# Kernel optimization log

Hardware: AMD Instinct MI355X
Metric: run time of the kernel (lower is better)

The kernel has to match this reference:

```python
import math
import jax, jax.numpy as jnp
import numpy as np

LN_2PI = math.log(2.0 * math.pi)


def _patches(x, K, s):
    # x: (N,1,h,w) -> (N,K*K,oh,ow); channel i*K+j is the (i,j)-shifted strided slice
    N, _, h, w = x.shape
    oh = (h - K) // s + 1
    ow = (w - K) // s + 1
    cols = [x[:, 0, i:i + s * (oh - 1) + 1:s, j:j + s * (ow - 1) + 1:s]
            for i in range(K) for j in range(K)]
    return jnp.stack(cols, axis=1)


def _em_routing(a, V, beta_a, beta_u, max_iter, C):
    # a: (b,ni,nj), V: (b,ni,nj,16)
    b, ni, nj, _ = V.shape
    ba = jnp.tile(beta_a, nj // C)[None, None, :]            # (1,1,nj)
    bu = jnp.tile(beta_u, nj // C)[None, None, :, None]      # (1,1,nj,1)
    R = jnp.full((b, ni, nj), 1.0 / nj, dtype=V.dtype)
    a_out = None
    miu = None
    for t in range(max_iter):
        lam = 0.01 * (1.0 - 0.95 ** (t + 1))
        R4 = (R * a)[..., None]                              # (b,ni,nj,1)
        coeff = jnp.maximum(R4.sum(1, keepdims=True), 1e-8)  # (b,1,nj,1)
        R4 = R4 / coeff
        miu = (R4 * V).sum(1, keepdims=True)                 # (b,1,nj,16)
        d2 = (V - miu) ** 2
        sigma = jnp.maximum((R4 * d2).sum(1, keepdims=True), 1e-8)
        log_sigma = jnp.log(sigma)
        cost = (bu + 0.5 * log_sigma) * coeff                # (b,1,nj,16)
        a_out = jax.nn.sigmoid(lam * (ba - cost.sum(-1)))    # (b,1,nj)
        if t != max_iter - 1:
            logp = -0.5 * (LN_2PI + log_sigma + d2 / sigma).sum(-1)  # (b,ni,nj)
            R = jax.nn.softmax(a_out * logp, axis=-1)
    return a_out[:, 0], miu[:, 0]


def _conv_capsule(a, M, W, beta_a, beta_u, B, C, K, stride, iters,
                  share=False, add_coord=False):
    bB, _, h, w = a.shape
    b = bB // B
    oh = (h - K) // stride + 1
    ow = (w - K) // stride + 1
    KK = K * K
    # pose patches -> (b,B,KK,1,oh*ow,4,4)
    Mp = _patches(M, K, stride).reshape(b, B, 4, 4, KK, 1, oh * ow)
    Mp = jnp.transpose(Mp, (0, 1, 4, 5, 6, 2, 3))
    if share:
        V = W[None, :, None, :, None] @ Mp                   # (b,B,KK,C,ohw,4,4)
    else:
        V = W[None, :, :, :, None] @ Mp
    if add_coord:
        ii = np.repeat(np.arange(K), K).astype(np.float32)
        jj = np.tile(np.arange(K), K).astype(np.float32)
        ll = np.repeat(np.arange(oh), ow).astype(np.float32)
        kk = np.tile(np.arange(ow), oh).astype(np.float32)
        pos_x = (stride * kk[None, :] + ii[:, None]) / w
        pos_y = (stride * ll[None, :] + jj[:, None]) / h
        coords = jnp.asarray(np.stack([pos_x, pos_y], -1))   # (KK,ohw,2)
        V = V.at[:, :, :, :, :, 0, :2].add(coords[None, None, :, None, :, :].astype(V.dtype))
    ap = _patches(a, K, stride).reshape(b, B * KK, oh * ow)
    a_i = jnp.tile(ap, (1, 1, C))                            # (b,B*KK,C*ohw)
    Vf = V.reshape(b, B * KK, C * oh * ow, 16)
    a_j, M_j = _em_routing(a_i, Vf, beta_a, beta_u, iters, C)
    a_out = a_j.reshape(b * C, 1, oh, ow)
    # faithful to original: permute(0,2,1) then flat view -> (b*C*16,1,oh,ow)
    M_out = jnp.transpose(M_j, (0, 2, 1)).reshape(b * C * 16, 1, oh, ow)
    return a_out, M_out


def setup_inputs() -> dict:
    key = jax.random.key(0)
    ks = jax.random.split(key, 16)
    f32 = jnp.float32
    eye = jnp.eye(4, dtype=f32)
    inp = {
        "x": jax.random.normal(ks[0], (16, 2, 32, 32), dtype=f32),
        "conv_w": 0.015 * jax.random.normal(ks[1], (32, 2, 5, 5), dtype=f32),
        "conv_b": jnp.zeros((32,), dtype=f32),
        "pose_w": 0.01 * jax.random.normal(ks[2], (512, 32), dtype=f32),
        "pose_b": jnp.zeros((512,), dtype=f32),
        "act_w": 0.01 * jax.random.normal(ks[3], (32, 32), dtype=f32),
        "act_b": jnp.zeros((32,), dtype=f32),
        "W2": eye[None, None] + jax.random.uniform(ks[4], (32, 9, 32, 4, 4), dtype=f32, minval=-0.03, maxval=0.03),
        "beta_a2": 0.1 * jax.random.normal(ks[5], (32,), dtype=f32),
        "beta_u2": 0.1 * jax.random.normal(ks[6], (32,), dtype=f32),
        "W3": eye[None, None] + jax.random.uniform(ks[7], (32, 9, 32, 4, 4), dtype=f32, minval=-0.03, maxval=0.03),
        "beta_a3": 0.1 * jax.random.normal(ks[8], (32,), dtype=f32),
        "beta_u3": 0.1 * jax.random.normal(ks[9], (32,), dtype=f32),
        "W4": eye[None] + jax.random.uniform(ks[10], (32, 5, 4, 4), dtype=f32, minval=-0.03, maxval=0.03),
        "beta_a4": 0.1 * jax.random.normal(ks[11], (5,), dtype=f32),
        "beta_u4": 0.1 * jax.random.normal(ks[12], (5,), dtype=f32),
    }
    return inp


def reference(x, conv_w, conv_b, pose_w, pose_b, act_w, act_b,
              W2, beta_a2, beta_u2, W3, beta_a3, beta_u3, W4, beta_a4, beta_u4):
    # stem conv 5x5 stride 2 + relu: (b,2,32,32) -> (b,32,14,14)
    fea = jax.lax.conv_general_dilated(
        x, conv_w, window_strides=(2, 2), padding="VALID",
        dimension_numbers=("NCHW", "OIHW", "NCHW")) + conv_b[None, :, None, None]
    fea = jax.nn.relu(fea)
    # primary capsules (1x1 convs)
    M = jnp.einsum("bchw,oc->bohw", fea, pose_w) + pose_b[None, :, None, None]
    a = jax.nn.sigmoid(jnp.einsum("bchw,oc->bohw", fea, act_w) + act_b[None, :, None, None])
    bsz, _, h, w = a.shape
    a = a.reshape(-1, 1, h, w)      # (b*32,1,14,14)
    M = M.reshape(-1, 1, h, w)      # (b*512,1,14,14)
    a, M = _conv_capsule(a, M, W2, beta_a2, beta_u2, B=32, C=32, K=3, stride=2, iters=3)
    a, M = _conv_capsule(a, M, W3, beta_a3, beta_u3, B=32, C=32, K=3, stride=1, iters=3)
    a, _ = _conv_capsule(a, M, W4, beta_a4, beta_u4, B=32, C=5, K=4, stride=1, iters=3,
                         share=True, add_coord=True)
    return a.reshape(x.shape[0], 5)
```

## Files before the change

kernel.cpp:

```cpp
#include <hip/hip_runtime.h>
#include <math.h>

#define LN2PI 1.83787706640934548356f

__global__ void k_stem(const float* __restrict__ x, const float* __restrict__ w,
                       const float* __restrict__ bias, float* __restrict__ fea) {
    int idx = blockIdx.x * blockDim.x + threadIdx.x;
    if (idx >= 16*32*14*14) return;
    int ox = idx % 14, oy = (idx/14) % 14, oc = (idx/196) % 32, b = idx/(196*32);
    float s = bias[oc];
    const float* xb = x + b*2*1024;
    const float* wc = w + oc*2*25;
    #pragma unroll
    for (int ic = 0; ic < 2; ++ic)
        #pragma unroll
        for (int ky = 0; ky < 5; ++ky)
            #pragma unroll
            for (int kx = 0; kx < 5; ++kx)
                s = fmaf(xb[ic*1024 + (oy*2+ky)*32 + (ox*2+kx)],
                         wc[ic*25 + ky*5 + kx], s);
    fea[idx] = fmaxf(s, 0.f);
}

__global__ void k_primary(const float* __restrict__ fea,
                          const float* __restrict__ pw, const float* __restrict__ pb,
                          const float* __restrict__ aw, const float* __restrict__ ab,
                          float* __restrict__ M, float* __restrict__ a) {
    int idx = blockIdx.x * blockDim.x + threadIdx.x;
    if (idx >= 16*544*196) return;
    int hw = idx % 196, o = (idx/196) % 544, b = idx/(196*544);
    const float* f = fea + b*32*196 + hw;
    if (o < 512) {
        float s = pb[o];
        #pragma unroll
        for (int c = 0; c < 32; ++c) s = fmaf(f[c*196], pw[o*32+c], s);
        M[(b*512+o)*196 + hw] = s;
    } else {
        int oo = o - 512;
        float s = ab[oo];
        #pragma unroll
        for (int c = 0; c < 32; ++c) s = fmaf(f[c*196], aw[oo*32+c], s);
        a[(b*32+oo)*196 + hw] = 1.f/(1.f + __expf(-s));
    }
}

__global__ void k_patch(const float* __restrict__ a_in, const float* __restrict__ M_in,
                        float* __restrict__ aP, float4* __restrict__ MpV,
                        int B, int K, int stride, int h, int w, int oh, int ow) {
    int P = oh*ow, KK = K*K, ni = B*KK;
    int idx = blockIdx.x * blockDim.x + threadIdx.x;
    if (idx >= 16*ni*P) return;
    int i = idx % ni, p = (idx/ni) % P, b = idx/(ni*P);
    int Bi = i / KK, kk = i % KK, ki = kk / K, kj = kk % K;
    int py = p / ow, px = p % ow;
    int src = (py*stride + ki)*w + (px*stride + kj);
    int hw = h*w;
    aP[idx] = a_in[(b*B + Bi)*hw + src];
    const float* Ms = M_in + (size_t)((b*B + Bi)*16)*hw + src;
    size_t base = (size_t)(b*P + p)*4;
    #pragma unroll
    for (int m4 = 0; m4 < 4; ++m4)
        MpV[(base + m4)*ni + i] = make_float4(Ms[(4*m4+0)*hw], Ms[(4*m4+1)*hw],
                                              Ms[(4*m4+2)*hw], Ms[(4*m4+3)*hw]);
}

__global__ void k_wt(const float* __restrict__ W, float4* __restrict__ WtV,
                     int NI, int C) {
    int idx = blockIdx.x * blockDim.x + threadIdx.x;
    if (idx >= NI*C) return;
    int i = idx % NI, c = idx/NI;
    const float* src = W + (size_t)(i*C + c)*16;
    #pragma unroll
    for (int m4 = 0; m4 < 4; ++m4)
        WtV[((size_t)c*4 + m4)*NI + i] = make_float4(src[4*m4+0], src[4*m4+1],
                                                     src[4*m4+2], src[4*m4+3]);
}

template<int NI, int NJ, int P, int C>
__global__ __launch_bounds__(256)
void k_stats(const float* __restrict__ aP, const float4* __restrict__ MpV,
             const float4* __restrict__ WtV, const float* __restrict__ svb,
             const float* __restrict__ mxs, const float* __restrict__ ism,
             const float* __restrict__ beta_a, const float* __restrict__ beta_u,
             float* __restrict__ statP,
             float* __restrict__ a_fin, float* __restrict__ M_fin,
             int t, float lam, int fin)
{
    constexpr int NIT = (NI + 63) / 64;
    constexpr int RS = 20;
    __shared__ float sRed[4][33*RS];
    int wave = threadIdx.x >> 6, lane = threadIdx.x & 63;
    int g  = blockIdx.x % (16*P);
    int cg = blockIdx.x / (16*P);
    int c  = cg*4 + wave;
    int bb = g / P, p = g % P;
    int j  = c*P + p;

    const float*  aPb = aP  + (size_t)(bb*P + p)*NI;
    const float4* Mb  = MpV + (size_t)(bb*P + p)*4*NI;
    const float4* Wb  = WtV + (size_t)c*4*NI;
    const float*  svr = svb + (size_t)(bb*NJ + j)*NI;
    const float*  mxb = mxs + bb*NI;
    const float*  imb = ism + bb*NI;

    float accw = 0.f, accm[16], acc2[16];
    #pragma unroll
    for (int m = 0; m < 16; ++m) { accm[m] = 0.f; acc2[m] = 0.f; }

    for (int it = 0; it < NIT; ++it) {
        int i = lane + it*64;
        if ((NI % 64 == 0) || (i < NI)) {
            float r;
            if (t == 0) r = 1.f / NJ;
            else        r = __expf(svr[i] - mxb[i]) * imb[i];
            float wgt = r * aPb[i];
            float4 m0 = Mb[0*NI + i], m1 = Mb[1*NI + i];
            float4 m2 = Mb[2*NI + i], m3 = Mb[3*NI + i];
            accw += wgt;
            #pragma unroll
            for (int rr = 0; rr < 4; ++rr) {
                float4 w = Wb[rr*NI + i];
                float v0 = fmaf(w.w, m3.x, fmaf(w.z, m2.x, fmaf(w.y, m1.x, w.x*m0.x)));
                float v1 = fmaf(w.w, m3.y, fmaf(w.z, m2.y, fmaf(w.y, m1.y, w.x*m0.y)));
                float v2 = fmaf(w.w, m3.z, fmaf(w.z, m2.z, fmaf(w.y, m1.z, w.x*m0.z)));
                float v3 = fmaf(w.w, m3.w, fmaf(w.z, m2.w, fmaf(w.y, m1.w, w.x*m0.w)));
                float t0 = wgt*v0, t1 = wgt*v1, t2 = wgt*v2, t3 = wgt*v3;
                accm[rr*4+0] += t0; acc2[rr*4+0] = fmaf(t0, v0, acc2[rr*4+0]);
                accm[rr*4+1] += t1; acc2[rr*4+1] = fmaf(t1, v1, acc2[rr*4+1]);
                accm[rr*4+2] += t2; acc2[rr*4+2] = fmaf(t2, v2, acc2[rr*4+2]);
                accm[rr*4+3] += t3; acc2[rr*4+3] = fmaf(t3, v3, acc2[rr*4+3]);
            }
        }
    }

    accw += __shfl_xor(accw, 1); accw += __shfl_xor(accw, 2);
    #pragma unroll
    for (int m = 0; m < 16; ++m) {
        accm[m] += __shfl_xor(accm[m], 1); accm[m] += __shfl_xor(accm[m], 2);
        acc2[m] += __shfl_xor(acc2[m], 1); acc2[m] += __shfl_xor(acc2[m], 2);
    }
    float* row = sRed[wave];
    if ((lane & 3) == 0) {
        int grp = lane >> 2;
        row[0*RS + grp] = accw;
        #pragma unroll
        for (int m = 0; m < 16; ++m) {
            row[(1+m)*RS + grp]  = accm[m];
            row[(17+m)*RS + grp] = acc2[m];
        }
    }
    float S = 0.f;
    if (lane < 33) {
        const float4* r4 = (const float4*)(row + lane*RS);
        float4 a = r4[0], b4 = r4[1], c4 = r4[2], d4 = r4[3];
        S = (((a.x+a.y)+(a.z+a.w)) + ((b4.x+b4.y)+(b4.z+b4.w)))
          + (((c4.x+c4.y)+(c4.z+c4.w)) + ((d4.x+d4.y)+(d4.z+d4.w)));
    }
    float coeff = fmaxf(__shfl(S, 0), 1e-8f);
    float Sn = S / coeff;
    bool sig_lane = (lane >= 17 && lane < 33);
    int src = sig_lane ? (lane - 16) : 0;
    float muk = __shfl(Sn, src);
    float lg = 0.f, iv = 0.f;
    if (sig_lane) {
        float s = fmaxf(Sn - muk*muk, 1e-8f);
        lg = __logf(s);
        iv = 1.f / s;
    }
    float v = sig_lane ? lg : 0.f;
    #pragma unroll
    for (int off = 1; off < 64; off <<= 1) v += __shfl_xor(v, off);
    float lsum = v;
    float ao = 1.f/(1.f + __expf(-(lam * (beta_a[j % C] - (16.f*beta_u[j % C] + 0.5f*lsum) * coeff))));
    float G = 0.f, H2 = 0.f, gmu2 = 0.f;
    if (sig_lane) {
        G = -0.5f*ao*iv;
        H2 = -2.f*G*muk;
        gmu2 = G*muk*muk;
    }
    float u = sig_lane ? gmu2 : 0.f;
    #pragma unroll
    for (int off = 1; off < 64; off <<= 1) u += __shfl_xor(u, off);
    float K1 = fmaf(-0.5f*ao, 16.f*LN2PI + lsum, u);

    float* st = statP + (size_t)(bb*NJ + j)*36;
    if (sig_lane) {
        st[lane-17]      = G;
        st[16 + lane-17] = H2;
    }
    if (lane == 0) st[32] = K1;
    if (fin) {
        if (lane == 0) a_fin[bb*NJ + j] = ao;
        if (lane >= 1 && lane < 17)
            M_fin[(size_t)(bb*16 + lane-1)*NJ + j] = Sn;
    }
}

template<int NI, int NJ, int P, int C, int NH>
__global__ __launch_bounds__(320)
void k_sv(const float4* __restrict__ MpV, const float4* __restrict__ WtV,
          const float* __restrict__ statP,
          float* __restrict__ svb, float* __restrict__ pmx, float* __restrict__ psm)
{
    constexpr int CH = C / NH;
    int p  = blockIdx.x % P;
    int bb = (blockIdx.x / P) % 16;
    int h  = blockIdx.x / (P*16);
    int i = threadIdx.x;
    bool act = (i < NI);

    float4 m0, m1, m2, m3;
    if (act) {
        const float4* Mb = MpV + (size_t)(bb*P + p)*4*NI;
        m0 = Mb[0*NI+i]; m1 = Mb[1*NI+i]; m2 = Mb[2*NI+i]; m3 = Mb[3*NI+i];
    }
    float mx = -3.0e38f, sm = 0.f;

    for (int cc = 0; cc < CH; ++cc) {
        int c = h*CH + cc;
        int j = c*P + p;
        const float* st = statP + (size_t)(bb*NJ + j)*36;
        if (act) {
            const float4* Wb = WtV + (size_t)c*4*NI;
            float4 w0 = Wb[0*NI+i], w1 = Wb[1*NI+i], w2 = Wb[2*NI+i], w3 = Wb[3*NI+i];
            float V[16];
            {
                float4 w = w0;
                V[0] = fmaf(w.w, m3.x, fmaf(w.z, m2.x, fmaf(w.y, m1.x, w.x*m0.x)));
                V[1] = fmaf(w.w, m3.y, fmaf(w.z, m2.y, fmaf(w.y, m1.y, w.x*m0.y)));
                V[2] = fmaf(w.w, m3.z, fmaf(w.z, m2.z, fmaf(w.y, m1.z, w.x*m0.z)));
                V[3] = fmaf(w.w, m3.w, fmaf(w.z, m2.w, fmaf(w.y, m1.w, w.x*m0.w)));
                w = w1;
                V[4] = fmaf(w.w, m3.x, fmaf(w.z, m2.x, fmaf(w.y, m1.x, w.x*m0.x)));
                V[5] = fmaf(w.w, m3.y, fmaf(w.z, m2.y, fmaf(w.y, m1.y, w.x*m0.y)));
                V[6] = fmaf(w.w, m3.z, fmaf(w.z, m2.z, fmaf(w.y, m1.z, w.x*m0.z)));
                V[7] = fmaf(w.w, m3.w, fmaf(w.z, m2.w, fmaf(w.y, m1.w, w.x*m0.w)));
                w = w2;
                V[8]  = fmaf(w.w, m3.x, fmaf(w.z, m2.x, fmaf(w.y, m1.x, w.x*m0.x)));
                V[9]  = fmaf(w.w, m3.y, fmaf(w.z, m2.y, fmaf(w.y, m1.y, w.x*m0.y)));
                V[10] = fmaf(w.w, m3.z, fmaf(w.z, m2.z, fmaf(w.y, m1.z, w.x*m0.z)));
                V[11] = fmaf(w.w, m3.w, fmaf(w.z, m2.w, fmaf(w.y, m1.w, w.x*m0.w)));
                w = w3;
                V[12] = fmaf(w.w, m3.x, fmaf(w.z, m2.x, fmaf(w.y, m1.x, w.x*m0.x)));
                V[13] = fmaf(w.w, m3.y, fmaf(w.z, m2.y, fmaf(w.y, m1.y, w.x*m0.y)));
                V[14] = fmaf(w.w, m3.z, fmaf(w.z, m2.z, fmaf(w.y, m1.z, w.x*m0.z)));
                V[15] = fmaf(w.w, m3.w, fmaf(w.z, m2.w, fmaf(w.y, m1.w, w.x*m0.w)));
            }
            float acc = 0.f;
            #pragma unroll
            for (int m = 0; m < 16; ++m) {
                float tmp = fmaf(V[m], st[m], st[16+m]);
                acc = fmaf(V[m], tmp, acc);
            }
            float sv = st[32] + acc;
            if (sv > mx) { sm = sm*__expf(mx - sv) + 1.f; mx = sv; }
            else         { sm += __expf(sv - mx); }
            svb[(size_t)(bb*NJ + j)*NI + i] = sv;
        }
    }
    if (act) {
        pmx[(size_t)(h*P + p)*(16*NI) + bb*NI + i] = mx;
        psm[(size_t)(h*P + p)*(16*NI) + bb*NI + i] = sm;
    }
}

__global__ void k_comb(const float* __restrict__ pmx, const float* __restrict__ psm,
                       float* __restrict__ mxs, float* __restrict__ ism,
                       int nch, int ntot)
{
    int idx = blockIdx.x * blockDim.x + threadIdx.x;
    if (idx >= ntot) return;
    float mx = -3.0e38f, sm = 0.f;
    for (int ch = 0; ch < nch; ++ch) {
        float m2 = pmx[(size_t)ch*ntot + idx];
        float s2 = psm[(size_t)ch*ntot + idx];
        float M = fmaxf(mx, m2);
        sm = sm*__expf(mx - M) + s2*__expf(m2 - M);
        mx = M;
    }
    mxs[idx] = mx;
    ism[idx] = 1.f / sm;
}

__global__ __launch_bounds__(512)
void k_layer4(const float* __restrict__ a3, const float* __restrict__ M3,
              const float* __restrict__ W4, const float* __restrict__ ba4,
              const float* __restrict__ bu4, float* __restrict__ out)
{
    __shared__ float sMt[16*512];
    __shared__ float sA[512];
    __shared__ float sW[2560];
    __shared__ float sR[2560];
    __shared__ float sStat[5][34];

    int b = blockIdx.x, tid = threadIdx.x;
    int lane = tid & 63, wave = tid >> 6;

    for (int k = tid; k < 8192; k += 512) {
        int i = k & 511, m = k >> 9;
        sMt[k] = M3[b*8192 + (i & ~15)*16 + m*16 + (i & 15)];
    }
    sA[tid] = a3[b*512 + tid];
    for (int k = tid; k < 2560; k += 512) { sW[k] = W4[k]; sR[k] = 0.2f; }
    __syncthreads();

    const float lams[3] = {5.0e-4f, 9.75e-4f, 1.426250e-3f};

    for (int t = 0; t < 3; ++t) {
        if (wave < 5) {
            int j = wave;
            float accw = 0.f, accm[16], acc2[16];
            #pragma unroll
            for (int m = 0; m < 16; ++m) { accm[m] = 0.f; acc2[m] = 0.f; }
            for (int u = 0; u < 8; ++u) {
                int i = u*64 + lane;
                float wgt = sR[i*5 + j] * sA[i];
                float Mm[16];
                #pragma unroll
                for (int m = 0; m < 16; ++m) Mm[m] = sMt[m*512 + i];
                const float* Wm = &sW[((i>>4)*5 + j)*16];
                float V[16];
                #pragma unroll
                for (int r = 0; r < 4; ++r)
                    #pragma unroll
                    for (int cc = 0; cc < 4; ++cc) {
                        float s = Wm[r*4+0]*Mm[0*4+cc];
                        s = fmaf(Wm[r*4+1], Mm[1*4+cc], s);
                        s = fmaf(Wm[r*4+2], Mm[2*4+cc], s);
                        s = fmaf(Wm[r*4+3], Mm[3*4+cc], s);
                        V[r*4+cc] = s;
                    }
                V[0] += (float)((i & 15) >> 2) * 0.25f;
                V[1] += (float)(i & 3) * 0.25f;
                accw += wgt;
                #pragma unroll
                for (int m = 0; m < 16; ++m) {
                    float t1 = wgt * V[m];
                    accm[m] += t1;
                    acc2[m] = fmaf(t1, V[m], acc2[m]);
                }
            }
            for (int off = 1; off < 64; off <<= 1) {
                accw += __shfl_xor(accw, off);
                #pragma unroll
                for (int m = 0; m < 16; ++m) accm[m] += __shfl_xor(accm[m], off);
                #pragma unroll
                for (int m = 0; m < 16; ++m) acc2[m] += __shfl_xor(acc2[m], off);
            }
            float coeff = fmaxf(accw, 1e-8f);
            float lsum = 0.f, mu[16], isv[16];
            #pragma unroll
            for (int m = 0; m < 16; ++m) {
                mu[m] = accm[m] / coeff;
                float s = fmaxf(acc2[m]/coeff - mu[m]*mu[m], 1e-8f);
                lsum += __logf(s);
                isv[m] = 1.f / s;
            }
            float ao = 1.f/(1.f + __expf(-(lams[t] * (ba4[j] - (16.f*bu4[j] + 0.5f*lsum) * coeff))));
            if (lane == 0) {
                #pragma unroll
                for (int m = 0; m < 16; ++m) { sStat[j][m] = mu[m]; sStat[j][16+m] = isv[m]; }
                sStat[j][32] = lsum; sStat[j][33] = ao;
            }
        }
        __syncthreads();
        if (t < 2) {
            int i = tid;
            float Mm[16];
            #pragma unroll
            for (int m = 0; m < 16; ++m) Mm[m] = sMt[m*512 + i];
            float sv[5], mxv = -3.0e38f;
            #pragma unroll
            for (int j = 0; j < 5; ++j) {
                const float* Wm = &sW[((i>>4)*5 + j)*16];
                float V[16];
                #pragma unroll
                for (int r = 0; r < 4; ++r)
                    #pragma unroll
                    for (int cc = 0; cc < 4; ++cc) {
                        float s = Wm[r*4+0]*Mm[0*4+cc];
                        s = fmaf(Wm[r*4+1], Mm[1*4+cc], s);
                        s = fmaf(Wm[r*4+2], Mm[2*4+cc], s);
                        s = fmaf(Wm[r*4+3], Mm[3*4+cc], s);
                        V[r*4+cc] = s;
                    }
                V[0] += (float)((i & 15) >> 2) * 0.25f;
                V[1] += (float)(i & 3) * 0.25f;
                float q = 0.f;
                #pragma unroll
                for (int m = 0; m < 16; ++m) {
                    float d = V[m] - sStat[j][m];
                    q = fmaf(d*d, sStat[j][16+m], q);
                }
                float logp = -0.5f * (16.f*LN2PI + sStat[j][32] + q);
                sv[j] = sStat[j][33] * logp;
                mxv = fmaxf(mxv, sv[j]);
            }
            float sum = 0.f;
            #pragma unroll
            for (int j = 0; j < 5; ++j) { sv[j] = __expf(sv[j] - mxv); sum += sv[j]; }
            float inv = 1.f / sum;
            #pragma unroll
            for (int j = 0; j < 5; ++j) sR[i*5 + j] = sv[j] * inv;
            __syncthreads();
        }
    }
    if (tid < 5) out[b*5 + tid] = sStat[tid][33];
}

template<int NI, int NJ, int P, int C, int NH>
static void run_em(hipStream_t stream,
                   const float* aP, const float4* MpV, const float4* WtV,
                   const float* ba, const float* bu,
                   float* statP, float* svb, float* mxs, float* ism,
                   float* pmx, float* psm,
                   float* a_fin, float* M_fin)
{
    const float lams[3] = {5.0e-4f, 9.75e-4f, 1.426250e-3f};
    for (int t = 0; t < 3; ++t) {
        k_stats<NI,NJ,P,C><<<16*NJ/4, 256, 0, stream>>>(
            aP, MpV, WtV, svb, mxs, ism, ba, bu, statP, a_fin, M_fin,
            t, lams[t], (t == 2) ? 1 : 0);
        if (t < 2) {
            k_sv<NI,NJ,P,C,NH><<<16*P*NH, 320, 0, stream>>>(MpV, WtV, statP, svb, pmx, psm);
            k_comb<<<(16*NI + 255)/256, 256, 0, stream>>>(pmx, psm, mxs, ism, NH*P, 16*NI);
        }
    }
}

extern "C" void kernel_launch(void* const* d_in, const int* in_sizes, int n_in,
                              void* d_out, int out_size, void* d_ws, size_t ws_size,
                              hipStream_t stream) {
    (void)in_sizes; (void)n_in; (void)out_size; (void)ws_size;
    const float* x       = (const float*)d_in[0];
    const float* conv_w  = (const float*)d_in[1];
    const float* conv_b  = (const float*)d_in[2];
    const float* pose_w  = (const float*)d_in[3];
    const float* pose_b  = (const float*)d_in[4];
    const float* act_w   = (const float*)d_in[5];
    const float* act_b   = (const float*)d_in[6];
    const float* W2      = (const float*)d_in[7];
    const float* beta_a2 = (const float*)d_in[8];
    const float* beta_u2 = (const float*)d_in[9];
    const float* W3      = (const float*)d_in[10];
    const float* beta_a3 = (const float*)d_in[11];
    const float* beta_u3 = (const float*)d_in[12];
    const float* W4      = (const float*)d_in[13];
    const float* beta_a4 = (const float*)d_in[14];
    const float* beta_u4 = (const float*)d_in[15];

    float* ws    = (float*)d_ws;
    float* fea   = ws;
    float* a1    = fea   + 100352;
    float* M1    = a1    + 100352;
    float* aP    = M1    + 1605632;
    float* Mp    = aP    + 165888;
    float* Wt    = Mp    + 2654208;
    float* statP = Wt    + 147456;
    float* svb   = statP + 663552;
    float* mxs   = svb   + 5308416;
    float* ismb  = mxs   + 4608;
    float* pmx   = ismb  + 4608;
    float* psm   = pmx   + 331776;
    float* a2    = psm   + 331776;
    float* M2    = a2    + 18432;
    float* a3    = M2    + 294912;
    float* M3    = a3    + 8192;

    float4* MpV = (float4*)Mp;
    float4* WtV = (float4*)Wt;

    k_stem<<<(16*32*196 + 255)/256, 256, 0, stream>>>(x, conv_w, conv_b, fea);
    k_primary<<<(16*544*196 + 255)/256, 256, 0, stream>>>(fea, pose_w, pose_b,
                                                          act_w, act_b, M1, a1);

    k_patch<<<(16*288*36 + 255)/256, 256, 0, stream>>>(a1, M1, aP, MpV, 32, 3, 2, 14, 14, 6, 6);
    k_wt<<<(288*32 + 255)/256, 256, 0, stream>>>(W2, WtV, 288, 32);
    run_em<288,1152,36,32,2>(stream, aP, MpV, WtV, beta_a2, beta_u2,
                             statP, svb, mxs, ismb, pmx, psm, a2, M2);

    k_patch<<<(16*288*16 + 255)/256, 256, 0, stream>>>(a2, M2, aP, MpV, 32, 3, 1, 6, 6, 4, 4);
    k_wt<<<(288*32 + 255)/256, 256, 0, stream>>>(W3, WtV, 288, 32);
    run_em<288,512,16,32,4>(stream, aP, MpV, WtV, beta_a3, beta_u3,
                            statP, svb, mxs, ismb, pmx, psm, a3, M3);

    k_layer4<<<16, 512, 0, stream>>>(a3, M3, W4, beta_a4, beta_u4, (float*)d_out);
}
```

Before: 532.0 us.

## Split online softmax reduction out of k_sv into separate chunked kernel

k_sv no longer tracks the running max/sum online; it only computes and stores the logits. A new k_red kernel then re-reads svb in chunks of 64 j-values to produce partial max/sum, which k_comb combines. The head split (NH) is dropped, so k_sv launches fewer blocks that each loop over all C, and the exp work moves out of k_sv. In exchange svb is read an extra time and there is one more launch per iteration.

```diff
diff --git a/kernel.cpp b/kernel.cpp
--- a/kernel.cpp
+++ b/kernel.cpp
@@ -196,72 +196,75 @@
     }
 }
 
-template<int NI, int NJ, int P, int C, int NH>
+template<int NI, int NJ, int P, int C>
 __global__ __launch_bounds__(320)
 void k_sv(const float4* __restrict__ MpV, const float4* __restrict__ WtV,
-          const float* __restrict__ statP,
-          float* __restrict__ svb, float* __restrict__ pmx, float* __restrict__ psm)
-{
-    constexpr int CH = C / NH;
-    int p  = blockIdx.x % P;
-    int bb = (blockIdx.x / P) % 16;
-    int h  = blockIdx.x / (P*16);
+          const float* __restrict__ statP, float* __restrict__ svb)
+{
+    int p = blockIdx.x % P, bb = blockIdx.x / P;
     int i = threadIdx.x;
-    bool act = (i < NI);
-
-    float4 m0, m1, m2, m3;
-    if (act) {
-        const float4* Mb = MpV + (size_t)(bb*P + p)*4*NI;
-        m0 = Mb[0*NI+i]; m1 = Mb[1*NI+i]; m2 = Mb[2*NI+i]; m3 = Mb[3*NI+i];
-    }
-    float mx = -3.0e38f, sm = 0.f;
-
-    for (int cc = 0; cc < CH; ++cc) {
-        int c = h*CH + cc;
+    if (i >= NI) return;
+
+    const float4* Mb = MpV + (size_t)(bb*P + p)*4*NI;
+    float4 m0 = Mb[0*NI+i], m1 = Mb[1*NI+i], m2 = Mb[2*NI+i], m3 = Mb[3*NI+i];
+
+    for (int c = 0; c < C; ++c) {
         int j = c*P + p;
         const float* st = statP + (size_t)(bb*NJ + j)*36;
-        if (act) {
-            const float4* Wb = WtV + (size_t)c*4*NI;
-            float4 w0 = Wb[0*NI+i], w1 = Wb[1*NI+i], w2 = Wb[2*NI+i], w3 = Wb[3*NI+i];
-            float V[16];
-            {
-                float4 w = w0;
-                V[0] = fmaf(w.w, m3.x, fmaf(w.z, m2.x, fmaf(w.y, m1.x, w.x*m0.x)));
-                V[1] = fmaf(w.w, m3.y, fmaf(w.z, m2.y, fmaf(w.y, m1.y, w.x*m0.y)));
-                V[2] = fmaf(w.w, m3.z, fmaf(w.z, m2.z, fmaf(w.y, m1.z, w.x*m0.z)));
-                V[3] = fmaf(w.w, m3.w, fmaf(w.z, m2.w, fmaf(w.y, m1.w, w.x*m0.w)));
-                w = w1;
-                V[4] = fmaf(w.w, m3.x, fmaf(w.z, m2.x, fmaf(w.y, m1.x, w.x*m0.x)));
-                V[5] = fmaf(w.w, m3.y, fmaf(w.z, m2.y, fmaf(w.y, m1.y, w.x*m0.y)));
-                V[6] = fmaf(w.w, m3.z, fmaf(w.z, m2.z, fmaf(w.y, m1.z, w.x*m0.z)));
-                V[7] = fmaf(w.w, m3.w, fmaf(w.z, m2.w, fmaf(w.y, m1.w, w.x*m0.w)));
-                w = w2;
-                V[8]  = fmaf(w.w, m3.x, fmaf(w.z, m2.x, fmaf(w.y, m1.x, w.x*m0.x)));
-                V[9]  = fmaf(w.w, m3.y, fmaf(w.z, m2.y, fmaf(w.y, m1.y, w.x*m0.y)));
-                V[10] = fmaf(w.w, m3.z, fmaf(w.z, m2.z, fmaf(w.y, m1.z, w.x*m0.z)));
-                V[11] = fmaf(w.w, m3.w, fmaf(w.z, m2.w, fmaf(w.y, m1.w, w.x*m0.w)));
-                w = w3;
-                V[12] = fmaf(w.w, m3.x, fmaf(w.z, m2.x, fmaf(w.y, m1.x, w.x*m0.x)));
-                V[13] = fmaf(w.w, m3.y, fmaf(w.z, m2.y, fmaf(w.y, m1.y, w.x*m0.y)));
-                V[14] = fmaf(w.w, m3.z, fmaf(w.z, m2.z, fmaf(w.y, m1.z, w.x*m0.z)));
-                V[15] = fmaf(w.w, m3.w, fmaf(w.z, m2.w, fmaf(w.y, m1.w, w.x*m0.w)));
-            }
-            float acc = 0.f;
-            #pragma unroll
-            for (int m = 0; m < 16; ++m) {
-                float tmp = fmaf(V[m], st[m], st[16+m]);
-                acc = fmaf(V[m], tmp, acc);
-            }
-            float sv = st[32] + acc;
-            if (sv > mx) { sm = sm*__expf(mx - sv) + 1.f; mx = sv; }
-            else         { sm += __expf(sv - mx); }
-            svb[(size_t)(bb*NJ + j)*NI + i] = sv;
-        }
-    }
-    if (act) {
-        pmx[(size_t)(h*P + p)*(16*NI) + bb*NI + i] = mx;
-        psm[(size_t)(h*P + p)*(16*NI) + bb*NI + i] = sm;
-    }
+        const float4* Wb = WtV + (size_t)c*4*NI;
+        float4 w0 = Wb[0*NI+i], w1 = Wb[1*NI+i], w2 = Wb[2*NI+i], w3 = Wb[3*NI+i];
+        float V[16];
+        {
+            float4 w = w0;
+            V[0] = fmaf(w.w, m3.x, fmaf(w.z, m2.x, fmaf(w.y, m1.x, w.x*m0.x)));
+            V[1] = fmaf(w.w, m3.y, fmaf(w.z, m2.y, fmaf(w.y, m1.y, w.x*m0.y)));
+            V[2] = fmaf(w.w, m3.z, fmaf(w.z, m2.z, fmaf(w.y, m1.z, w.x*m0.z)));
+            V[3] = fmaf(w.w, m3.w, fmaf(w.z, m2.w, fmaf(w.y, m1.w, w.x*m0.w)));
+            w = w1;
+            V[4] = fmaf(w.w, m3.x, fmaf(w.z, m2.x, fmaf(w.y, m1.x, w.x*m0.x)));
+            V[5] = fmaf(w.w, m3.y, fmaf(w.z, m2.y, fmaf(w.y, m1.y, w.x*m0.y)));
+            V[6] = fmaf(w.w, m3.z, fmaf(w.z, m2.z, fmaf(w.y, m1.z, w.x*m0.z)));
+            V[7] = fmaf(w.w, m3.w, fmaf(w.z, m2.w, fmaf(w.y, m1.w, w.x*m0.w)));
+            w = w2;
+            V[8]  = fmaf(w.w, m3.x, fmaf(w.z, m2.x, fmaf(w.y, m1.x, w.x*m0.x)));
+            V[9]  = fmaf(w.w, m3.y, fmaf(w.z, m2.y, fmaf(w.y, m1.y, w.x*m0.y)));
+            V[10] = fmaf(w.w, m3.z, fmaf(w.z, m2.z, fmaf(w.y, m1.z, w.x*m0.z)));
+            V[11] = fmaf(w.w, m3.w, fmaf(w.z, m2.w, fmaf(w.y, m1.w, w.x*m0.w)));
+            w = w3;
+            V[12] = fmaf(w.w, m3.x, fmaf(w.z, m2.x, fmaf(w.y, m1.x, w.x*m0.x)));
+            V[13] = fmaf(w.w, m3.y, fmaf(w.z, m2.y, fmaf(w.y, m1.y, w.x*m0.y)));
+            V[14] = fmaf(w.w, m3.z, fmaf(w.z, m2.z, fmaf(w.y, m1.z, w.x*m0.z)));
+            V[15] = fmaf(w.w, m3.w, fmaf(w.z, m2.w, fmaf(w.y, m1.w, w.x*m0.w)));
+        }
+        float acc = 0.f;
+        #pragma unroll
+        for (int m = 0; m < 16; ++m) {
+            float tmp = fmaf(V[m], st[m], st[16+m]);
+            acc = fmaf(V[m], tmp, acc);
+        }
+        svb[(size_t)(bb*NJ + j)*NI + i] = st[32] + acc;
+    }
+}
+
+template<int NI, int NJ, int JCH>
+__global__ void k_red(const float* __restrict__ svb,
+                      float* __restrict__ pmx, float* __restrict__ psm)
+{
+    constexpr int NCH = NJ / JCH;
+    int idx = blockIdx.x * blockDim.x + threadIdx.x;
+    if (idx >= 16*NI*NCH) return;
+    int i  = idx % NI;
+    int bb = (idx / NI) % 16;
+    int ch = idx / (NI*16);
+    const float* base = svb + (size_t)bb*NJ*NI + (size_t)ch*JCH*NI + i;
+    float mx = -3.0e38f, sm = 0.f;
+    for (int k = 0; k < JCH; ++k) {
+        float v = base[(size_t)k*NI];
+        if (v > mx) { sm = sm*__expf(mx - v) + 1.f; mx = v; }
+        else        { sm += __expf(v - mx); }
+    }
+    pmx[(size_t)ch*(16*NI) + bb*NI + i] = mx;
+    psm[(size_t)ch*(16*NI) + bb*NI + i] = sm;
 }
 
 __global__ void k_comb(const float* __restrict__ pmx, const float* __restrict__ psm,
@@ -408,7 +411,7 @@
     if (tid < 5) out[b*5 + tid] = sStat[tid][33];
 }
 
-template<int NI, int NJ, int P, int C, int NH>
+template<int NI, int NJ, int P, int C>
 static void run_em(hipStream_t stream,
                    const float* aP, const float4* MpV, const float4* WtV,
                    const float* ba, const float* bu,
@@ -416,14 +419,17 @@
                    float* pmx, float* psm,
                    float* a_fin, float* M_fin)
 {
+    constexpr int JCH = 64;
+    constexpr int NCH = NJ / JCH;
     const float lams[3] = {5.0e-4f, 9.75e-4f, 1.426250e-3f};
     for (int t = 0; t < 3; ++t) {
         k_stats<NI,NJ,P,C><<<16*NJ/4, 256, 0, stream>>>(
             aP, MpV, WtV, svb, mxs, ism, ba, bu, statP, a_fin, M_fin,
             t, lams[t], (t == 2) ? 1 : 0);
         if (t < 2) {
-            k_sv<NI,NJ,P,C,NH><<<16*P*NH, 320, 0, stream>>>(MpV, WtV, statP, svb, pmx, psm);
-            k_comb<<<(16*NI + 255)/256, 256, 0, stream>>>(pmx, psm, mxs, ism, NH*P, 16*NI);
+            k_sv<NI,NJ,P,C><<<16*P, 320, 0, stream>>>(MpV, WtV, statP, svb);
+            k_red<NI,NJ,JCH><<<(16*NI*NCH + 255)/256, 256, 0, stream>>>(svb, pmx, psm);
+            k_comb<<<(16*NI + 255)/256, 256, 0, stream>>>(pmx, psm, mxs, ism, NCH, 16*NI);
         }
     }
 }
@@ -476,13 +482,13 @@
 
     k_patch<<<(16*288*36 + 255)/256, 256, 0, stream>>>(a1, M1, aP, MpV, 32, 3, 2, 14, 14, 6, 6);
     k_wt<<<(288*32 + 255)/256, 256, 0, stream>>>(W2, WtV, 288, 32);
-    run_em<288,1152,36,32,2>(stream, aP, MpV, WtV, beta_a2, beta_u2,
-                             statP, svb, mxs, ismb, pmx, psm, a2, M2);
+    run_em<288,1152,36,32>(stream, aP, MpV, WtV, beta_a2, beta_u2,
+                           statP, svb, mxs, ismb, pmx, psm, a2, M2);
 
     k_patch<<<(16*288*16 + 255)/256, 256, 0, stream>>>(a2, M2, aP, MpV, 32, 3, 1, 6, 6, 4, 4);
     k_wt<<<(288*32 + 255)/256, 256, 0, stream>>>(W3, WtV, 288, 32);
-    run_em<288,512,16,32,4>(stream, aP, MpV, WtV, beta_a3, beta_u3,
-                            statP, svb, mxs, ismb, pmx, psm, a3, M3);
+    run_em<288,512,16,32>(stream, aP, MpV, WtV, beta_a3, beta_u3,
+                          statP, svb, mxs, ismb, pmx, psm, a3, M3);
 
     k_layer4<<<16, 512, 0, stream>>>(a3, M3, W4, beta_a4, beta_u4, (float*)d_out);
 }
```

Result: slower. 546.6 us (+2.8%).

## Software-prefetch k_stats loads and drop the output-split in k_sv

Applied to the files above, without the earlier changes.

k_stats now loads the next 64-wide slice of M, W, activations and routing terms into registers while computing on the current slice. The loop is fully unrolled, out-of-range lanes use a clamped index and a zero mask, and a waves-per-eu attribute is added. k_sv no longer splits the C output capsules across NH blocks; each block loops over all C, so the partial buffers and k_comb shrink by NH. This reduces the partial-combine traffic and hides load latency, but k_sv has fewer blocks and more serial work per block, which lowers parallelism, and the prefetch raises register pressure.

```diff
diff --git a/kernel.cpp b/kernel.cpp
--- a/kernel.cpp
+++ b/kernel.cpp
@@ -77,7 +77,7 @@
 }
 
 template<int NI, int NJ, int P, int C>
-__global__ __launch_bounds__(256)
+__global__ __launch_bounds__(256) __attribute__((amdgpu_waves_per_eu(4,8)))
 void k_stats(const float* __restrict__ aP, const float4* __restrict__ MpV,
              const float4* __restrict__ WtV, const float* __restrict__ svb,
              const float* __restrict__ mxs, const float* __restrict__ ism,
@@ -107,29 +107,49 @@
     #pragma unroll
     for (int m = 0; m < 16; ++m) { accm[m] = 0.f; acc2[m] = 0.f; }
 
+    int iC = (lane < NI) ? lane : (NI-1);
+    float4 mc0 = Mb[0*NI+iC], mc1 = Mb[1*NI+iC], mc2 = Mb[2*NI+iC], mc3 = Mb[3*NI+iC];
+    float4 wc0 = Wb[0*NI+iC], wc1 = Wb[1*NI+iC], wc2 = Wb[2*NI+iC], wc3 = Wb[3*NI+iC];
+    float apc = aPb[iC];
+    float svc = 0.f, mxc = 0.f, imc = 0.f;
+    if (t > 0) { svc = svr[iC]; mxc = mxb[iC]; imc = imb[iC]; }
+
+    #pragma unroll
     for (int it = 0; it < NIT; ++it) {
-        int i = lane + it*64;
-        if ((NI % 64 == 0) || (i < NI)) {
-            float r;
-            if (t == 0) r = 1.f / NJ;
-            else        r = __expf(svr[i] - mxb[i]) * imb[i];
-            float wgt = r * aPb[i];
-            float4 m0 = Mb[0*NI + i], m1 = Mb[1*NI + i];
-            float4 m2 = Mb[2*NI + i], m3 = Mb[3*NI + i];
+        float4 mn0, mn1, mn2, mn3, wn0, wn1, wn2, wn3;
+        float apn = 0.f, svn = 0.f, mxn = 0.f, imn = 0.f;
+        if (it + 1 < NIT) {
+            int i = lane + (it+1)*64;
+            int iN = (i < NI) ? i : (NI-1);
+            mn0 = Mb[0*NI+iN]; mn1 = Mb[1*NI+iN]; mn2 = Mb[2*NI+iN]; mn3 = Mb[3*NI+iN];
+            wn0 = Wb[0*NI+iN]; wn1 = Wb[1*NI+iN]; wn2 = Wb[2*NI+iN]; wn3 = Wb[3*NI+iN];
+            apn = aPb[iN];
+            if (t > 0) { svn = svr[iN]; mxn = mxb[iN]; imn = imb[iN]; }
+        }
+        {
+            int i = lane + it*64;
+            float mask = ((NI % 64 == 0) || (i < NI)) ? 1.f : 0.f;
+            float r = (t == 0) ? (1.f/NJ) : (__expf(svc - mxc) * imc);
+            float wgt = r * apc * mask;
             accw += wgt;
             #pragma unroll
             for (int rr = 0; rr < 4; ++rr) {
-                float4 w = Wb[rr*NI + i];
-                float v0 = fmaf(w.w, m3.x, fmaf(w.z, m2.x, fmaf(w.y, m1.x, w.x*m0.x)));
-                float v1 = fmaf(w.w, m3.y, fmaf(w.z, m2.y, fmaf(w.y, m1.y, w.x*m0.y)));
-                float v2 = fmaf(w.w, m3.z, fmaf(w.z, m2.z, fmaf(w.y, m1.z, w.x*m0.z)));
-                float v3 = fmaf(w.w, m3.w, fmaf(w.z, m2.w, fmaf(w.y, m1.w, w.x*m0.w)));
+                float4 w = (rr == 0) ? wc0 : (rr == 1) ? wc1 : (rr == 2) ? wc2 : wc3;
+                float v0 = fmaf(w.w, mc3.x, fmaf(w.z, mc2.x, fmaf(w.y, mc1.x, w.x*mc0.x)));
+                float v1 = fmaf(w.w, mc3.y, fmaf(w.z, mc2.y, fmaf(w.y, mc1.y, w.x*mc0.y)));
+                float v2 = fmaf(w.w, mc3.z, fmaf(w.z, mc2.z, fmaf(w.y, mc1.z, w.x*mc0.z)));
+                float v3 = fmaf(w.w, mc3.w, fmaf(w.z, mc2.w, fmaf(w.y, mc1.w, w.x*mc0.w)));
                 float t0 = wgt*v0, t1 = wgt*v1, t2 = wgt*v2, t3 = wgt*v3;
                 accm[rr*4+0] += t0; acc2[rr*4+0] = fmaf(t0, v0, acc2[rr*4+0]);
                 accm[rr*4+1] += t1; acc2[rr*4+1] = fmaf(t1, v1, acc2[rr*4+1]);
                 accm[rr*4+2] += t2; acc2[rr*4+2] = fmaf(t2, v2, acc2[rr*4+2]);
                 accm[rr*4+3] += t3; acc2[rr*4+3] = fmaf(t3, v3, acc2[rr*4+3]);
             }
+        }
+        if (it + 1 < NIT) {
+            mc0 = mn0; mc1 = mn1; mc2 = mn2; mc3 = mn3;
+            wc0 = wn0; wc1 = wn1; wc2 = wn2; wc3 = wn3;
+            apc = apn; svc = svn; mxc = mxn; imc = imn;
         }
     }
 
@@ -159,8 +179,8 @@
     float coeff = fmaxf(__shfl(S, 0), 1e-8f);
     float Sn = S / coeff;
     bool sig_lane = (lane >= 17 && lane < 33);
-    int src = sig_lane ? (lane - 16) : 0;
-    float muk = __shfl(Sn, src);
+    int srcl = sig_lane ? (lane - 16) : 0;
+    float muk = __shfl(Sn, srcl);
     float lg = 0.f, iv = 0.f;
     if (sig_lane) {
         float s = fmaxf(Sn - muk*muk, 1e-8f);
@@ -196,16 +216,13 @@
     }
 }
 
-template<int NI, int NJ, int P, int C, int NH>
+template<int NI, int NJ, int P, int C>
 __global__ __launch_bounds__(320)
 void k_sv(const float4* __restrict__ MpV, const float4* __restrict__ WtV,
           const float* __restrict__ statP,
           float* __restrict__ svb, float* __restrict__ pmx, float* __restrict__ psm)
 {
-    constexpr int CH = C / NH;
-    int p  = blockIdx.x % P;
-    int bb = (blockIdx.x / P) % 16;
-    int h  = blockIdx.x / (P*16);
+    int p = blockIdx.x % P, bb = blockIdx.x / P;
     int i = threadIdx.x;
     bool act = (i < NI);
 
@@ -216,8 +233,7 @@
     }
     float mx = -3.0e38f, sm = 0.f;
 
-    for (int cc = 0; cc < CH; ++cc) {
-        int c = h*CH + cc;
+    for (int c = 0; c < C; ++c) {
         int j = c*P + p;
         const float* st = statP + (size_t)(bb*NJ + j)*36;
         if (act) {
@@ -259,8 +275,8 @@
         }
     }
     if (act) {
-        pmx[(size_t)(h*P + p)*(16*NI) + bb*NI + i] = mx;
-        psm[(size_t)(h*P + p)*(16*NI) + bb*NI + i] = sm;
+        pmx[(size_t)p*(16*NI) + bb*NI + i] = mx;
+        psm[(size_t)p*(16*NI) + bb*NI + i] = sm;
     }
 }
 
@@ -408,7 +424,7 @@
     if (tid < 5) out[b*5 + tid] = sStat[tid][33];
 }
 
-template<int NI, int NJ, int P, int C, int NH>
+template<int NI, int NJ, int P, int C>
 static void run_em(hipStream_t stream,
                    const float* aP, const float4* MpV, const float4* WtV,
                    const float* ba, const float* bu,
@@ -422,8 +438,8 @@
             aP, MpV, WtV, svb, mxs, ism, ba, bu, statP, a_fin, M_fin,
             t, lams[t], (t == 2) ? 1 : 0);
         if (t < 2) {
-            k_sv<NI,NJ,P,C,NH><<<16*P*NH, 320, 0, stream>>>(MpV, WtV, statP, svb, pmx, psm);
-            k_comb<<<(16*NI + 255)/256, 256, 0, stream>>>(pmx, psm, mxs, ism, NH*P, 16*NI);
+            k_sv<NI,NJ,P,C><<<16*P, 320, 0, stream>>>(MpV, WtV, statP, svb, pmx, psm);
+            k_comb<<<(16*NI + 255)/256, 256, 0, stream>>>(pmx, psm, mxs, ism, P, 16*NI);
         }
     }
 }
@@ -476,13 +492,13 @@
 
     k_patch<<<(16*288*36 + 255)/256, 256, 0, stream>>>(a1, M1, aP, MpV, 32, 3, 2, 14, 14, 6, 6);
     k_wt<<<(288*32 + 255)/256, 256, 0, stream>>>(W2, WtV, 288, 32);
-    run_em<288,1152,36,32,2>(stream, aP, MpV, WtV, beta_a2, beta_u2,
-                             statP, svb, mxs, ismb, pmx, psm, a2, M2);
+    run_em<288,1152,36,32>(stream, aP, MpV, WtV, beta_a2, beta_u2,
+                           statP, svb, mxs, ismb, pmx, psm, a2, M2);
 
     k_patch<<<(16*288*16 + 255)/256, 256, 0, stream>>>(a2, M2, aP, MpV, 32, 3, 1, 6, 6, 4, 4);
     k_wt<<<(288*32 + 255)/256, 256, 0, stream>>>(W3, WtV, 288, 32);
-    run_em<288,512,16,32,4>(stream, aP, MpV, WtV, beta_a3, beta_u3,
-                            statP, svb, mxs, ismb, pmx, psm, a3, M3);
+    run_em<288,512,16,32>(stream, aP, MpV, WtV, beta_a3, beta_u3,
+                          statP, svb, mxs, ismb, pmx, psm, a3, M3);
 
     k_layer4<<<16, 512, 0, stream>>>(a3, M3, W4, beta_a4, beta_u4, (float*)d_out);
 }
```

After: 883.4 us. +66.1%, slower.
